# Optimization experiments

Measured on AMD Instinct MI355X. Metric: run time of the kernel, lower is better.

Reference implementation:

```python
import jax, jax.numpy as jnp
import numpy as np
from jax import lax

WS = 0.1  # brevitas SignedBinaryWeightPerTensorConst scaling constant

def bq(w):
    # signed binary weight quant (sign * const scale) with straight-through estimator
    return w + lax.stop_gradient(WS * jnp.where(w >= 0, 1.0, -1.0) - w)

def bact(x):
    # QuantHardTanh with SignedBinaryActPerTensorConst (scale 1.0): clamp then binarize (STE)
    y = jnp.clip(x, -1.0, 1.0)
    return y + lax.stop_gradient(jnp.where(y >= 0, 1.0, -1.0) - y)

def conv1d(x, wq, b, dil):
    # x: [N,C,L], wq: [O,I,K] (already quantized), VALID padding, stride 1, rhs dilation
    y = lax.conv_general_dilated(x, wq, window_strides=(1,), padding='VALID',
                                 rhs_dilation=(dil,), dimension_numbers=('NCH', 'OIH', 'NCH'))
    return y + b[None, :, None]

def mp(x, k, p):
    # MaxPool1d(kernel=k, stride=k, padding=p)
    return lax.reduce_window(x, -jnp.inf, lax.max, (1, 1, k), (1, 1, k),
                             ((0, 0), (0, 0), (p, p)))

def sb(x, w, b):
    # QuantScaleBias: per-channel binary-quantized scale + float bias
    return x * bq(w)[None, :, None] + b[None, :, None]

def setup_inputs() -> dict:
    key = jax.random.key(0)
    ks = jax.random.split(key, 32)
    C, D = 256, 8
    def n(k, shape, s=1.0):
        return jax.random.normal(k, shape, jnp.float32) * s
    inp = {"x": n(ks[0], (128, 3, 2560))}
    specs = [(3, C, 23), (C, C, 13), (C, C, 7), (C, C, 5), (C, C, 5), (C, D, 3)]
    i = 1
    for li, (ci, co, k) in enumerate(specs, start=1):
        inp[f"w{li}"] = n(ks[i], (co, ci, k), 0.1)
        inp[f"b{li}"] = n(ks[i + 1], (co,), 0.01)
        inp[f"sw{li}"] = n(ks[i + 2], (co,))
        inp[f"sb{li}"] = n(ks[i + 3], (co,), 0.01)
        i += 4
    inp["fw1"] = n(ks[25], (512, 32), 0.1)
    inp["fsw1"] = n(ks[26], (512,))
    inp["fsb1"] = n(ks[27], (512,), 0.01)
    inp["fw2"] = n(ks[28], (1000, 512), 0.1)
    inp["fsw2"] = n(ks[29], (1000,))
    inp["fsb2"] = n(ks[30], (1000,), 0.01)
    return inp

def reference(x, w1, b1, sw1, sb1, w2, b2, sw2, sb2, w3, b3, sw3, sb3,
              w4, b4, sw4, sb4, w5, b5, sw5, sb5, w6, b6, sw6, sb6,
              fw1, fsw1, fsb1, fw2, fsw2, fsb2):
    x = bact(sb(mp(conv1d(x, bq(w1), b1, 7), 5, 2), sw1, sb1))  # L: 2560->2406->482
    x = bact(sb(mp(conv1d(x, bq(w2), b2, 3), 3, 1), sw2, sb2))  # ->446->149
    x = bact(sb(mp(conv1d(x, bq(w3), b3, 2), 3, 1), sw3, sb3))  # ->137->46
    x = bact(sb(conv1d(x, bq(w4), b4, 1), sw4, sb4))            # ->42
    x = bact(sb(mp(conv1d(x, bq(w5), b5, 1), 3, 1), sw5, sb5))  # ->38->13
    x = bact(sb(mp(conv1d(x, bq(w6), b6, 1), 3, 1), sw6, sb6))  # ->11->4, C=8
    x = x.reshape(-1, 32)  # depth * embedding_factor = 8*4
    x = x @ bq(fw1).T
    x = bact(x * bq(fsw1) + fsb1)
    x = x @ bq(fw2).T
    return x * bq(fsw2) + fsb2
```

## Files before the change

kernel.cpp:

```cpp
#include <hip/hip_runtime.h>
#include <cstdint>
#include <cstddef>

typedef unsigned long long u64;
typedef uint32_t u32;
typedef uint16_t u16;
typedef uint8_t u8;
typedef __attribute__((ext_vector_type(8))) short bf16x8;
typedef __attribute__((ext_vector_type(4))) float f32x4;


#define CONV1_MARGIN 1e-4f

struct PackJob { const float* src; u64* dst; int Cout, CIN, K, waveBase; };
struct PackJobs {
    PackJob j[6]; int totalWaves;
    const float* fw1; u32* fw1pk;
    const float* w1;  u16* wbf;
};

__global__ void pack_all_kernel(PackJobs P)
{
    int gtid = blockIdx.x * blockDim.x + threadIdx.x;
    int wid = gtid >> 6, lane = gtid & 63;
    if (wid < P.totalWaves) {
        int jj = 0;
        #pragma unroll
        for (int i = 1; i < 6; ++i) if (wid >= P.j[i].waveBase) jj = i;
        PackJob job = P.j[jj];
        int lw = wid - job.waveBase;
        int W = job.CIN >> 6;
        int wg = lw % W;
        int co = (lw / W) % job.Cout;
        int k  = lw / (W * job.Cout);
        int ci = wg * 64 + lane;
        bool sg = job.src[((size_t)co * job.CIN + ci) * job.K + k] >= 0.0f;
        u64 word = __ballot(sg);
        if (lane == 0) job.dst[lw] = word;
        return;
    }
    int idx = gtid - P.totalWaves * 64;
    if (idx < 512) {
        u32 wd = 0;
        #pragma unroll
        for (int i = 0; i < 32; ++i) wd |= (u32)(P.fw1[idx * 32 + i] >= 0.0f) << i;
        P.fw1pk[idx] = wd;
    }
    int j = idx - 512;
    if (j >= 0 && j < 256 * 192) {
        int co = j / 192, k = j - co * 192;
        int i = (k >= 96) ? (k - 96) : k;
        u16 val = 0;
        if (i < 69)
            val = (P.w1[(size_t)co * 69 + i] >= 0.0f) ? (u16)0x3F80 : (u16)0xBF80;
        P.wbf[(size_t)co * 192 + k] = val;
    }
}

__global__ __launch_bounds__(256) void conv1_mfma_kernel(
    const float* __restrict__ x, const u16* __restrict__ wbf,
    const float* __restrict__ b, const float* __restrict__ sw,
    const float* __restrict__ sb,
    u64* __restrict__ opk64, u64* __restrict__ uflag64)
{
    __shared__ u32 xhl[3 * 236];
    __shared__ u32 Xb32[16 * 108];
    __shared__ float poolf[128 * 81];
    const int Lconv = 2406, Lin = 2560;
    int n = blockIdx.x, T = blockIdx.y, ch = blockIdx.z;
    int tid = threadIdx.x, lane = tid & 63, w = tid >> 6;
    int l0 = 80 * T - 2;

    bf16x8 afr[2][6];
    {
        int cobase = 128 * ch + 32 * w;
        #pragma unroll
        for (int m = 0; m < 2; ++m) {
            const u16* wp = wbf + (size_t)(cobase + m * 16 + (lane & 15)) * 192
                           + (lane >> 4) * 8;
            #pragma unroll
            for (int s = 0; s < 6; ++s)
                afr[m][s] = *(const bf16x8*)(wp + s * 32);
        }
    }

    const float* xb = x + (size_t)n * 3 * Lin;
    #pragma unroll
    for (int e = 0; e < 3; ++e) {
        int idx = tid + 256 * e;
        if (idx < 3 * 236) {
            int ci = idx / 236, lrel = idx - ci * 236;
            int l = min(max(l0 + lrel, 0), Lin - 1);
            float xv = xb[ci * Lin + l];
            u32 ub = __float_as_uint(xv);
            u32 h = (ub + 0x7FFFu + ((ub >> 16) & 1u)) >> 16;
            float rem = xv - __uint_as_float(h << 16);
            u32 ur = __float_as_uint(rem);
            u32 lo = (ur + 0x7FFFu + ((ur >> 16) & 1u)) >> 16;
            xhl[idx] = (h & 0xFFFFu) | (lo << 16);
        }
    }
    __syncthreads();

    for (int j = 0; j < 5; ++j) {
        if (j) __syncthreads();
        #pragma unroll
        for (int e = 0; e < 3; ++e) {
            int s = tid + 256 * e;
            int p = s & 15, i2 = s >> 4;
            u32 hiw = 0, low = 0;
            #pragma unroll
            for (int t2 = 0; t2 < 2; ++t2) {
                int t = 2 * i2 + t2;
                if (t < 69) {
                    int ci = (t < 23) ? 0 : ((t < 46) ? 1 : 2);
                    int kk = t - 23 * ci;
                    u32 v = xhl[ci * 236 + 16 * j + p + 7 * kk];
                    hiw |= (v & 0xFFFFu) << (16 * t2);
                    low |= (v >> 16) << (16 * t2);
                }
            }
            Xb32[p * 108 + i2] = hiw;
            Xb32[p * 108 + 48 + i2] = low;
        }
        __syncthreads();

        f32x4 acc0 = {0.0f, 0.0f, 0.0f, 0.0f};
        f32x4 acc1 = {0.0f, 0.0f, 0.0f, 0.0f};
        const u16* brow = (const u16*)Xb32 + (lane & 15) * 216 + (lane >> 4) * 8;
        #pragma unroll
        for (int s = 0; s < 6; ++s) {
            bf16x8 bf = *(const bf16x8*)(brow + s * 32);
            acc0 = __builtin_amdgcn_mfma_f32_16x16x32_bf16(afr[0][s], bf, acc0, 0, 0, 0);
            acc1 = __builtin_amdgcn_mfma_f32_16x16x32_bf16(afr[1][s], bf, acc1, 0, 0, 0);
        }

        int q = 16 * j + (lane & 15);
        #pragma unroll
        for (int m = 0; m < 2; ++m) {
            #pragma unroll
            for (int r = 0; r < 4; ++r) {
                float v = (m == 0) ? acc0[r] : acc1[r];
                int co_loc = 32 * w + 16 * m + (lane >> 4) * 4 + r;
                poolf[co_loc * 81 + q] = v;
            }
        }
    }
    __syncthreads();

    #pragma unroll
    for (int it = 0; it < 8; ++it) {
        int idx = tid + 256 * it;
        int co_loc = idx & 127;
        int lp_loc = idx >> 7;
        int lp = 16 * T + lp_loc;
        int co = 128 * ch + co_loc;
        bool bit = false, unc = false;
        if (lp < 482) {
            float best = -1e30f;
            #pragma unroll
            for (int t = 0; t < 5; ++t) {
                int q = 5 * lp_loc + t;
                int l = l0 + q;
                if (l >= 0 && l < Lconv)
                    best = fmaxf(best, poolf[co_loc * 81 + q]);
            }
            float v = ((sw[co] >= 0.0f) ? 0.1f : -0.1f) * (0.1f * best + b[co]) + sb[co];
            bit = (v >= 0.0f);
            unc = (fabsf(v) < CONV1_MARGIN);
        }
        u64 wb = __ballot(bit);
        u64 wu = __ballot(unc);
        if (lp < 482 && lane == 0) {
            size_t widx = ((size_t)n * 482 + lp) * 4 + (ch * 2 + (co_loc >> 6));
            opk64[widx] = wb;
            uflag64[widx] = wu;
        }
    }
}

__global__ void conv1_fixup_kernel(const float* __restrict__ x,
                                   const float* __restrict__ w1,
                                   const float* __restrict__ b,
                                   const float* __restrict__ sw,
                                   const float* __restrict__ sb,
                                   const u64* __restrict__ uflag64,
                                   u64* __restrict__ opk64)
{
    int idx = blockIdx.x * blockDim.x + threadIdx.x;
    if (idx >= 128 * 482 * 4) return;
    u64 f = uflag64[idx];
    if (f == 0) return;
    int og = idx & 3;
    int lp = (idx >> 2) % 482;
    int n = idx / (4 * 482);
    u64 word = opk64[idx];
    const float* xb = x + (size_t)n * 3 * 2560;
    while (f) {
        int c = __ffsll(f) - 1;
        f &= f - 1;
        int co = og * 64 + c;
        const float* wp = w1 + (size_t)co * 69;
        double best = -1e300;
        for (int t = 0; t < 5; ++t) {
            int gl = 5 * lp - 2 + t;
            if (gl < 0 || gl >= 2406) continue;
            double s = 0.0;
            #pragma unroll
            for (int ci = 0; ci < 3; ++ci) {
                const float* xp = xb + ci * 2560 + gl;
                const float* wq = wp + ci * 23;
                #pragma unroll
                for (int kk = 0; kk < 23; ++kk) {
                    double xv = (double)xp[kk * 7];
                    s += (wq[kk] >= 0.0f) ? xv : -xv;
                }
            }
            best = fmax(best, s);
        }
        double v = ((sw[co] >= 0.0f) ? 0.1 : -0.1) * (0.1 * best + (double)b[co]) + (double)sb[co];
        u64 bit = (v >= 0.0) ? 1ull : 0ull;
        word = (word & ~(1ull << c)) | (bit << c);
    }
    opk64[idx] = word;
}

template<int K, int DIL, int PK, int PP, int W, int LPW>
__global__ void bconv_bit_kernel(const u64* __restrict__ apk,
                                 const u64* __restrict__ wpk,
                                 const float* __restrict__ b,
                                 const float* __restrict__ sw,
                                 const float* __restrict__ sb,
                                 u64* __restrict__ opk,
                                 int Cout, int Lin, int Lconv, int Lout,
                                 int NLPG, int nwaves)
{
    int wid = __builtin_amdgcn_readfirstlane(
        (int)(blockIdx.x * (blockDim.x >> 6)) + (int)(threadIdx.x >> 6));
    int lane = threadIdx.x & 63;
    if (wid >= nwaves) return;
    int WOUT = Cout >> 6;
    int og = wid % WOUT;
    int lpg = (wid / WOUT) % NLPG;
    int n  = wid / (WOUT * NLPG);
    int lp0 = lpg * LPW;
    int co = og * 64 + lane;

    const u64* ab = apk + (size_t)n * Lin * W;
    int cnt[LPW][PK];
    #pragma unroll
    for (int j = 0; j < LPW; ++j)
        #pragma unroll
        for (int t = 0; t < PK; ++t) cnt[j][t] = 0;

    #pragma unroll
    for (int k = 0; k < K; ++k) {
        u64 ww[W];
        #pragma unroll
        for (int w = 0; w < W; ++w)
            ww[w] = wpk[((size_t)k * Cout + co) * W + w];
        #pragma unroll
        for (int j = 0; j < LPW; ++j) {
            int lp = lp0 + j;
            #pragma unroll
            for (int t = 0; t < PK; ++t) {
                int l = lp * PK - PP + t;
                if (lp >= Lout || l < 0 || l >= Lconv) continue;
                const u64* ap = ab + (size_t)(l + k * DIL) * W;
                #pragma unroll
                for (int w = 0; w < W; ++w)
                    cnt[j][t] += __popcll(ap[w] ^ ww[w]);
            }
        }
    }
    const int CINK = W * 64 * K;
    #pragma unroll
    for (int j = 0; j < LPW; ++j) {
        int lp = lp0 + j;
        int best = -2147483647;
        #pragma unroll
        for (int t = 0; t < PK; ++t) {
            int l = lp * PK - PP + t;
            if (l < 0 || l >= Lconv) continue;
            int ksum = CINK - 2 * cnt[j][t];
            best = (ksum > best) ? ksum : best;
        }
        bool bit = false;
        if (lp < Lout) {
            double conv = 0.1 * (double)best + (double)b[co];
            double v = ((sw[co] >= 0.0f) ? 0.1 : -0.1) * conv + (double)sb[co];
            bit = (v >= 0.0);
        }
        u64 word = __ballot(bit);
        if (lp < Lout && lane == 0)
            opk[((size_t)n * Lout + lp) * WOUT + og] = word;
    }
}

__global__ __launch_bounds__(256) void tail_kernel(
    const u64* __restrict__ a3,
    const u64* __restrict__ wpk4,
    const u64* __restrict__ wpk5,
    const u64* __restrict__ wpk6,
    const float* __restrict__ b4, const float* __restrict__ sw4, const float* __restrict__ sb4,
    const float* __restrict__ b5, const float* __restrict__ sw5, const float* __restrict__ sb5,
    const float* __restrict__ b6, const float* __restrict__ sw6, const float* __restrict__ sb6,
    const u32* __restrict__ fw1pk,
    const float* __restrict__ fsw1, const float* __restrict__ fsb1,
    const u64* __restrict__ fpk2,
    const float* __restrict__ fsw2, const float* __restrict__ fsb2,
    float* __restrict__ out)
{
    __shared__ u64 sA[46 * 4];
    __shared__ u64 sB[42 * 4];
    __shared__ u64 sC[13 * 4];
    __shared__ u32 sA6;
    __shared__ u64 sH[8];
    int n = blockIdx.x, tid = threadIdx.x, lane = tid & 63, wv = tid >> 6;

    for (int i = tid; i < 46 * 4; i += 256) sA[i] = a3[(size_t)n * 46 * 4 + i];
    __syncthreads();

    {
        u64 ww[5][4];
        #pragma unroll
        for (int k = 0; k < 5; ++k)
            #pragma unroll
            for (int w = 0; w < 4; ++w)
                ww[k][w] = wpk4[((size_t)k * 256 + tid) * 4 + w];
        double bc = b4[tid];
        double swc = (sw4[tid] >= 0.0f) ? 0.1 : -0.1;
        double sbc = sb4[tid];
        for (int lp = 0; lp < 42; ++lp) {
            int cnt = 0;
            #pragma unroll
            for (int k = 0; k < 5; ++k)
                #pragma unroll
                for (int w = 0; w < 4; ++w)
                    cnt += __popcll(sA[(lp + k) * 4 + w] ^ ww[k][w]);
            int ksum = 256 * 5 - 2 * cnt;
            double v = swc * (0.1 * ksum + bc) + sbc;
            u64 word = __ballot(v >= 0.0);
            if (lane == 0) sB[lp * 4 + wv] = word;
        }
    }
    __syncthreads();

    {
        u64 ww[5][4];
        #pragma unroll
        for (int k = 0; k < 5; ++k)
            #pragma unroll
            for (int w = 0; w < 4; ++w)
                ww[k][w] = wpk5[((size_t)k * 256 + tid) * 4 + w];
        double bc = b5[tid];
        double swc = (sw5[tid] >= 0.0f) ? 0.1 : -0.1;
        double sbc = sb5[tid];
        for (int lp = 0; lp < 13; ++lp) {
            int best = -2147483647;
            #pragma unroll
            for (int t = 0; t < 3; ++t) {
                int l = 3 * lp - 1 + t;
                if (l < 0 || l >= 38) continue;
                int cnt = 0;
                #pragma unroll
                for (int k = 0; k < 5; ++k)
                    #pragma unroll
                    for (int w = 0; w < 4; ++w)
                        cnt += __popcll(sB[(l + k) * 4 + w] ^ ww[k][w]);
                int ksum = 256 * 5 - 2 * cnt;
                best = (ksum > best) ? ksum : best;
            }
            double v = swc * (0.1 * best + bc) + sbc;
            u64 word = __ballot(v >= 0.0);
            if (lane == 0) sC[lp * 4 + wv] = word;
        }
    }
    __syncthreads();

    if (tid < 32) {
        int co = tid >> 2, lp = tid & 3;
        int best = -2147483647;
        for (int t = 0; t < 3; ++t) {
            int l = 3 * lp - 1 + t;
            if (l < 0 || l >= 11) continue;
            int cnt = 0;
            #pragma unroll
            for (int k = 0; k < 3; ++k)
                #pragma unroll
                for (int w = 0; w < 4; ++w)
                    cnt += __popcll(sC[(l + k) * 4 + w] ^ wpk6[((size_t)k * 8 + co) * 4 + w]);
            int ksum = 256 * 3 - 2 * cnt;
            best = (ksum > best) ? ksum : best;
        }
        double v = ((sw6[co] >= 0.0f) ? 0.1 : -0.1) * (0.1 * best + (double)b6[co]) + (double)sb6[co];
        u64 word = __ballot(v >= 0.0);
        if (tid == 0) sA6 = (u32)word;
    }
    __syncthreads();

    {
        u32 a6w = sA6;
        #pragma unroll
        for (int p = 0; p < 2; ++p) {
            int o = tid + p * 256;
            int k = 32 - 2 * __popc(a6w ^ fw1pk[o]);
            double v = ((fsw1[o] >= 0.0f) ? 0.1 : -0.1) * (0.1 * (double)k) + (double)fsb1[o];
            u64 word = __ballot(v >= 0.0);
            if (lane == 0) sH[p * 4 + wv] = word;
        }
    }
    __syncthreads();

    {
        u64 h[8];
        #pragma unroll
        for (int w = 0; w < 8; ++w) h[w] = sH[w];
        #pragma unroll
        for (int p = 0; p < 4; ++p) {
            int o = tid + p * 256;
            if (o < 1000) {
                int cnt = 0;
                #pragma unroll
                for (int w = 0; w < 8; ++w)
                    cnt += __popcll(h[w] ^ fpk2[(size_t)o * 8 + w]);
                int k = 512 - 2 * cnt;
                double v = ((fsw2[o] >= 0.0f) ? 0.1 : -0.1) * (0.1 * (double)k) + (double)fsb2[o];
                out[(size_t)n * 1000 + o] = (float)v;
            }
        }
    }
}

extern "C" void kernel_launch(void* const* d_in, const int* in_sizes, int n_in,
                              void* d_out, int out_size, void* d_ws, size_t ws_size,
                              hipStream_t stream) {
    const float* x = (const float*)d_in[0];
    const float *w[6], *b[6], *sw[6], *sb[6];
    for (int i = 0; i < 6; ++i) {
        w[i]  = (const float*)d_in[1 + 4 * i];
        b[i]  = (const float*)d_in[2 + 4 * i];
        sw[i] = (const float*)d_in[3 + 4 * i];
        sb[i] = (const float*)d_in[4 + 4 * i];
    }
    const float* fw1  = (const float*)d_in[25];
    const float* fsw1 = (const float*)d_in[26];
    const float* fsb1 = (const float*)d_in[27];
    const float* fw2  = (const float*)d_in[28];
    const float* fsw2 = (const float*)d_in[29];
    const float* fsb2 = (const float*)d_in[30];
    float* out = (float*)d_out;
    (void)in_sizes; (void)n_in; (void)out_size; (void)ws_size;

    char* wsbase = (char*)d_ws;
    size_t off = 0;
    auto alloc = [&](size_t bytes) -> char* {
        char* p = wsbase + off;
        off = (off + bytes + 255) & ~(size_t)255;
        return p;
    };
    u64* wpk2 = (u64*)alloc((size_t)13 * 256 * 4 * 8);
    u64* wpk3 = (u64*)alloc((size_t)7 * 256 * 4 * 8);
    u64* wpk4 = (u64*)alloc((size_t)5 * 256 * 4 * 8);
    u64* wpk5 = (u64*)alloc((size_t)5 * 256 * 4 * 8);
    u64* wpk6 = (u64*)alloc((size_t)3 * 8 * 4 * 8);
    u64* fpk2 = (u64*)alloc((size_t)1000 * 8 * 8);
    u32* fw1pk = (u32*)alloc((size_t)512 * 4);
    u16* wbf = (u16*)alloc((size_t)256 * 192 * 2);
    u64* uflag64 = (u64*)alloc((size_t)128 * 482 * 4 * 8);
    u64* a1   = (u64*)alloc((size_t)128 * 482 * 4 * 8);
    u64* a2   = (u64*)alloc((size_t)128 * 149 * 4 * 8);
    u64* a3   = (u64*)alloc((size_t)128 * 46 * 4 * 8);

    const int BLK = 256;
    auto blocksForWaves = [](int nwaves) { return dim3((unsigned)((nwaves * 64 + 255) / 256)); };
    auto blocksForThreads = [](int n) { return dim3((unsigned)((n + 255) / 256)); };

    {
        PackJobs P;
        int base = 0;
        auto setJob = [&](int i, const float* src, u64* dst, int Cout, int CIN, int K) {
            P.j[i] = {src, dst, Cout, CIN, K, base};
            base += K * Cout * (CIN >> 6);
        };
        setJob(0, w[1], wpk2, 256, 256, 13);
        setJob(1, w[2], wpk3, 256, 256, 7);
        setJob(2, w[3], wpk4, 256, 256, 5);
        setJob(3, w[4], wpk5, 256, 256, 5);
        setJob(4, w[5], wpk6, 8, 256, 3);
        setJob(5, fw2, fpk2, 1000, 512, 1);
        P.totalWaves = base;
        P.fw1 = fw1; P.fw1pk = fw1pk; P.w1 = w[0]; P.wbf = wbf;
        int totalThreads = base * 64 + 512 + 256 * 192;
        pack_all_kernel<<<blocksForThreads(totalThreads), BLK, 0, stream>>>(P);
    }

    conv1_mfma_kernel<<<dim3(128, 31, 2), BLK, 0, stream>>>(
        x, wbf, b[0], sw[0], sb[0], a1, uflag64);
    conv1_fixup_kernel<<<blocksForThreads(128 * 482 * 4), BLK, 0, stream>>>(
        x, w[0], b[0], sw[0], sb[0], uflag64, a1);

    {
        const int NLPG = (149 + 3) / 4;
        int nw = 128 * NLPG * 4;
        bconv_bit_kernel<13, 3, 3, 1, 4, 4><<<blocksForWaves(nw), BLK, 0, stream>>>(
            a1, wpk2, b[1], sw[1], sb[1], a2, 256, 482, 446, 149, NLPG, nw);
    }
    {
        const int NLPG = (46 + 3) / 4;
        int nw = 128 * NLPG * 4;
        bconv_bit_kernel<7, 2, 3, 1, 4, 4><<<blocksForWaves(nw), BLK, 0, stream>>>(
            a2, wpk3, b[2], sw[2], sb[2], a3, 256, 149, 137, 46, NLPG, nw);
    }
    tail_kernel<<<dim3(128), BLK, 0, stream>>>(
        a3, wpk4, wpk5, wpk6,
        b[3], sw[3], sb[3], b[4], sw[4], sb[4], b[5], sw[5], sb[5],
        fw1pk, fsw1, fsb1, fpk2, fsw2, fsb2, out);
}
```

Measured before the change: 314.7 us.

## Split conv1 into 64-channel blocks and stage binary-conv activations in LDS

```diff
diff --git a/kernel.cpp b/kernel.cpp
--- a/kernel.cpp
+++ b/kernel.cpp
@@ -65,23 +65,19 @@
 {
     __shared__ u32 xhl[3 * 236];
     __shared__ u32 Xb32[16 * 108];
-    __shared__ float poolf[128 * 81];
+    __shared__ float poolf[64 * 81];
     const int Lconv = 2406, Lin = 2560;
     int n = blockIdx.x, T = blockIdx.y, ch = blockIdx.z;
     int tid = threadIdx.x, lane = tid & 63, w = tid >> 6;
     int l0 = 80 * T - 2;
 
-    bf16x8 afr[2][6];
+    bf16x8 afr[6];
     {
-        int cobase = 128 * ch + 32 * w;
-        #pragma unroll
-        for (int m = 0; m < 2; ++m) {
-            const u16* wp = wbf + (size_t)(cobase + m * 16 + (lane & 15)) * 192
-                           + (lane >> 4) * 8;
-            #pragma unroll
-            for (int s = 0; s < 6; ++s)
-                afr[m][s] = *(const bf16x8*)(wp + s * 32);
-        }
+        int cobase = 64 * ch + 16 * w;
+        const u16* wp = wbf + (size_t)(cobase + (lane & 15)) * 192 + (lane >> 4) * 8;
+        #pragma unroll
+        for (int s = 0; s < 6; ++s)
+            afr[s] = *(const bf16x8*)(wp + s * 32);
     }
 
     const float* xb = x + (size_t)n * 3 * Lin;
@@ -125,36 +121,30 @@
         }
         __syncthreads();
 
-        f32x4 acc0 = {0.0f, 0.0f, 0.0f, 0.0f};
-        f32x4 acc1 = {0.0f, 0.0f, 0.0f, 0.0f};
+        f32x4 acc = {0.0f, 0.0f, 0.0f, 0.0f};
         const u16* brow = (const u16*)Xb32 + (lane & 15) * 216 + (lane >> 4) * 8;
         #pragma unroll
         for (int s = 0; s < 6; ++s) {
             bf16x8 bf = *(const bf16x8*)(brow + s * 32);
-            acc0 = __builtin_amdgcn_mfma_f32_16x16x32_bf16(afr[0][s], bf, acc0, 0, 0, 0);
-            acc1 = __builtin_amdgcn_mfma_f32_16x16x32_bf16(afr[1][s], bf, acc1, 0, 0, 0);
+            acc = __builtin_amdgcn_mfma_f32_16x16x32_bf16(afr[s], bf, acc, 0, 0, 0);
         }
 
         int q = 16 * j + (lane & 15);
         #pragma unroll
-        for (int m = 0; m < 2; ++m) {
-            #pragma unroll
-            for (int r = 0; r < 4; ++r) {
-                float v = (m == 0) ? acc0[r] : acc1[r];
-                int co_loc = 32 * w + 16 * m + (lane >> 4) * 4 + r;
-                poolf[co_loc * 81 + q] = v;
-            }
+        for (int r = 0; r < 4; ++r) {
+            int co_loc = 16 * w + (lane >> 4) * 4 + r;
+            poolf[co_loc * 81 + q] = acc[r];
         }
     }
     __syncthreads();
 
     #pragma unroll
-    for (int it = 0; it < 8; ++it) {
+    for (int it = 0; it < 4; ++it) {
         int idx = tid + 256 * it;
-        int co_loc = idx & 127;
-        int lp_loc = idx >> 7;
+        int co_loc = idx & 63;
+        int lp_loc = idx >> 6;
         int lp = 16 * T + lp_loc;
-        int co = 128 * ch + co_loc;
+        int co = 64 * ch + co_loc;
         bool bit = false, unc = false;
         if (lp < 482) {
             float best = -1e30f;
@@ -172,7 +162,7 @@
         u64 wb = __ballot(bit);
         u64 wu = __ballot(unc);
         if (lp < 482 && lane == 0) {
-            size_t widx = ((size_t)n * 482 + lp) * 4 + (ch * 2 + (co_loc >> 6));
+            size_t widx = ((size_t)n * 482 + lp) * 4 + ch;
             opk64[widx] = wb;
             uflag64[widx] = wu;
         }
@@ -226,27 +216,31 @@
 }
 
 template<int K, int DIL, int PK, int PP, int W, int LPW>
-__global__ void bconv_bit_kernel(const u64* __restrict__ apk,
-                                 const u64* __restrict__ wpk,
-                                 const float* __restrict__ b,
-                                 const float* __restrict__ sw,
-                                 const float* __restrict__ sb,
-                                 u64* __restrict__ opk,
-                                 int Cout, int Lin, int Lconv, int Lout,
-                                 int NLPG, int nwaves)
+__global__ __launch_bounds__(256) void bconv_lds_kernel(
+    const u64* __restrict__ apk,
+    const u64* __restrict__ wpk,
+    const float* __restrict__ b,
+    const float* __restrict__ sw,
+    const float* __restrict__ sb,
+    u64* __restrict__ opk,
+    int Cout, int Lin, int Lconv, int Lout)
 {
-    int wid = __builtin_amdgcn_readfirstlane(
-        (int)(blockIdx.x * (blockDim.x >> 6)) + (int)(threadIdx.x >> 6));
-    int lane = threadIdx.x & 63;
-    if (wid >= nwaves) return;
+    constexpr int SPAN = (LPW * PK - 1) + (K - 1) * DIL + 1;
+    __shared__ u64 sAct[SPAN * W];
+    int n = blockIdx.x, lpg = blockIdx.y;
+    int tid = threadIdx.x, lane = tid & 63, og = tid >> 6;
+    int lp0 = lpg * LPW;
+    int lbase = lp0 * PK - PP;
     int WOUT = Cout >> 6;
-    int og = wid % WOUT;
-    int lpg = (wid / WOUT) % NLPG;
-    int n  = wid / (WOUT * NLPG);
-    int lp0 = lpg * LPW;
     int co = og * 64 + lane;
 
     const u64* ab = apk + (size_t)n * Lin * W;
+    for (int i = tid; i < SPAN * W; i += 256) {
+        int li = lbase + i / W;
+        sAct[i] = (li >= 0 && li < Lin) ? ab[(size_t)li * W + (i % W)] : 0ull;
+    }
+    __syncthreads();
+
     int cnt[LPW][PK];
     #pragma unroll
     for (int j = 0; j < LPW; ++j)
@@ -266,7 +260,7 @@
             for (int t = 0; t < PK; ++t) {
                 int l = lp * PK - PP + t;
                 if (lp >= Lout || l < 0 || l >= Lconv) continue;
-                const u64* ap = ab + (size_t)(l + k * DIL) * W;
+                const u64* ap = sAct + (size_t)(l + k * DIL - lbase) * W;
                 #pragma unroll
                 for (int w = 0; w < W; ++w)
                     cnt[j][t] += __popcll(ap[w] ^ ww[w]);
@@ -473,7 +467,6 @@
     u64* a3   = (u64*)alloc((size_t)128 * 46 * 4 * 8);
 
     const int BLK = 256;
-    auto blocksForWaves = [](int nwaves) { return dim3((unsigned)((nwaves * 64 + 255) / 256)); };
     auto blocksForThreads = [](int n) { return dim3((unsigned)((n + 255) / 256)); };
 
     {
@@ -495,23 +488,15 @@
         pack_all_kernel<<<blocksForThreads(totalThreads), BLK, 0, stream>>>(P);
     }
 
-    conv1_mfma_kernel<<<dim3(128, 31, 2), BLK, 0, stream>>>(
+    conv1_mfma_kernel<<<dim3(128, 31, 4), BLK, 0, stream>>>(
         x, wbf, b[0], sw[0], sb[0], a1, uflag64);
     conv1_fixup_kernel<<<blocksForThreads(128 * 482 * 4), BLK, 0, stream>>>(
         x, w[0], b[0], sw[0], sb[0], uflag64, a1);
 
-    {
-        const int NLPG = (149 + 3) / 4;
-        int nw = 128 * NLPG * 4;
-        bconv_bit_kernel<13, 3, 3, 1, 4, 4><<<blocksForWaves(nw), BLK, 0, stream>>>(
-            a1, wpk2, b[1], sw[1], sb[1], a2, 256, 482, 446, 149, NLPG, nw);
-    }
-    {
-        const int NLPG = (46 + 3) / 4;
-        int nw = 128 * NLPG * 4;
-        bconv_bit_kernel<7, 2, 3, 1, 4, 4><<<blocksForWaves(nw), BLK, 0, stream>>>(
-            a2, wpk3, b[2], sw[2], sb[2], a3, 256, 149, 137, 46, NLPG, nw);
-    }
+    bconv_lds_kernel<13, 3, 3, 1, 4, 4><<<dim3(128, (149 + 3) / 4), BLK, 0, stream>>>(
+        a1, wpk2, b[1], sw[1], sb[1], a2, 256, 482, 446, 149);
+    bconv_lds_kernel<7, 2, 3, 1, 4, 4><<<dim3(128, (46 + 3) / 4), BLK, 0, stream>>>(
+        a2, wpk3, b[2], sw[2], sb[2], a3, 256, 149, 137, 46);
     tail_kernel<<<dim3(128), BLK, 0, stream>>>(
         a3, wpk4, wpk5, wpk6,
         b[3], sw[3], sb[3], b[4], sw[4], sb[4], b[5], sw[5], sb[5],
```

After: 292.3 us. 7.1% less time.
